# Kernel tuning notes

Measured on AMD Instinct MI355X. Metric: run time of the kernel, lower is better.

Reference implementation:

```python
import jax, jax.numpy as jnp
import numpy as np

GN_GROUPS = 32
GN_EPS = 1e-5


def _conv3x3(x, w, b):
    # NCHW 3x3 conv, stride 1, pad 1
    y = jax.lax.conv_general_dilated(x, w, (1, 1), [(1, 1), (1, 1)],
                                     dimension_numbers=('NCHW', 'OIHW', 'NCHW'))
    return y + b[None, :, None, None]


def _bilinear(x, py, px):
    # x: [N,C,H,W]; py,px: [N,H,W] fractional sample coords; zeros outside.
    N, C, H, W = x.shape
    y0 = jnp.floor(py)
    x0 = jnp.floor(px)
    wy = py - y0
    wx = px - x0
    xf = x.reshape(N, C, H * W)
    out = jnp.zeros((N, C, H, W), x.dtype)
    corners = ((y0, x0, (1 - wy) * (1 - wx)),
               (y0, x0 + 1, (1 - wy) * wx),
               (y0 + 1, x0, wy * (1 - wx)),
               (y0 + 1, x0 + 1, wy * wx))
    for yy, xx, w in corners:
        valid = ((yy >= 0) & (yy <= H - 1) & (xx >= 0) & (xx <= W - 1)).astype(x.dtype)
        yi = jnp.clip(yy, 0, H - 1).astype(jnp.int32)
        xi = jnp.clip(xx, 0, W - 1).astype(jnp.int32)
        idx = (yi * W + xi).reshape(N, 1, H * W)
        g = jnp.take_along_axis(xf, idx, axis=2).reshape(N, C, H, W)
        out = out + g * (w * valid)[:, None]
    return out


def setup_inputs() -> dict:
    key = jax.random.key(0)
    ks = jax.random.split(key, 8)
    N, C, H, W = 4, 128, 160, 160
    s = 0.05
    return {
        'x': jax.random.normal(ks[0], (N, C, H, W), jnp.float32),
        'w_tm': jax.random.normal(ks[1], (4, C, 3, 3), jnp.float32) * s,
        'b_tm': jax.random.normal(ks[2], (4,), jnp.float32) * s,
        'w_tr': jax.random.normal(ks[3], (2, C, 3, 3), jnp.float32) * s,
        'b_tr': jax.random.normal(ks[4], (2,), jnp.float32) * s,
        'w_dcn': jax.random.normal(ks[5], (C, C, 3, 3), jnp.float32) * s,
        'gn_gamma': jnp.ones((C,), jnp.float32),
        'gn_beta': jnp.zeros((C,), jnp.float32),
    }


def reference(x, w_tm, b_tm, w_tr, b_tr, w_dcn, gn_gamma, gn_beta):
    N, C, H, W = x.shape
    Cout = w_dcn.shape[0]
    # regular 3x3 grid offsets: row0 = ky, row1 = kx, k ordered ky-major
    R = jnp.array([[-1., -1., -1., 0., 0., 0., 1., 1., 1.],
                   [-1., 0., 1., -1., 0., 1., -1., 0., 1.]], x.dtype)
    tm = _conv3x3(x, w_tm, b_tm)   # [N,4,H,W] -> per-pixel 2x2 affine
    tr = _conv3x3(x, w_tr, b_tr)   # [N,2,H,W] -> per-pixel (dy,dx) translation
    tmm = tm.transpose(0, 2, 3, 1).reshape(N, H, W, 2, 2)
    off = jnp.einsum('nhwij,jk->nhwik', tmm, R) - R  # [N,H,W,2,9]
    dy = off[:, :, :, 0, :] + tr[:, 0][..., None]    # [N,H,W,9]
    dx = off[:, :, :, 1, :] + tr[:, 1][..., None]
    hh = jnp.arange(H, dtype=x.dtype)[None, :, None, None]
    ww = jnp.arange(W, dtype=x.dtype)[None, None, :, None]
    kk = jnp.arange(9)
    ky = (kk // 3).astype(x.dtype)
    kx = (kk % 3).astype(x.dtype)
    py = hh - 1.0 + ky + dy  # stride=1, pad=1, dilation=1
    px = ww - 1.0 + kx + dx
    wk = w_dcn.reshape(Cout, C, 9)
    out = jnp.zeros((N, Cout, H, W), x.dtype)
    for k in range(9):  # fixed small loop over kernel points
        s = _bilinear(x, py[..., k], px[..., k])
        out = out + jnp.einsum('nchw,oc->nohw', s, wk[:, :, k])
    # GroupNorm
    og = out.reshape(N, GN_GROUPS, (Cout // GN_GROUPS) * H * W)
    mu = og.mean(axis=2, keepdims=True)
    var = og.var(axis=2, keepdims=True)
    og = (og - mu) * jax.lax.rsqrt(var + GN_EPS)
    out = og.reshape(N, Cout, H, W) * gn_gamma[None, :, None, None] + gn_beta[None, :, None, None]
    return jax.nn.relu(out + x)
```

## Files before the change

### kernel.cpp

```cpp
#include <hip/hip_runtime.h>
#include <hip/hip_fp16.h>
#include <math.h>

#define Hh 160
#define Ww 160
#define Cc 128
#define HW 25600
#define NPIX 102400

typedef __attribute__((ext_vector_type(8))) _Float16 half8;
typedef __attribute__((ext_vector_type(4))) float f32x4;
typedef __attribute__((ext_vector_type(4))) unsigned int u32x4;

union h2u { __half2 h; unsigned int u; };

#define WS_OFFS 0u
#define WS_WA   7372800u
#define WS_GSUM 7667712u
#define WS_GSQ  7668224u
#define WS_XT   7668736u
#define WS_RAW  33883136u

__global__ void wtrans_kernel(const float* __restrict__ w_dcn,
                              unsigned short* __restrict__ wA) {
    int idx = blockIdx.x * 256 + threadIdx.x;
    if (idx >= 9 * 128 * 128) return;
    int k = idx >> 14;
    int o = (idx >> 7) & 127;
    int c = idx & 127;
    wA[idx] = __half_as_ushort(__float2half(w_dcn[(o * 128 + c) * 9 + k]));
}

__global__ void __launch_bounds__(256) xpose_kernel(
    const float* __restrict__ x, unsigned short* __restrict__ xT) {
    __shared__ float L[128 * 65];
    int b = blockIdx.x;
    int n = b / 400;
    int px0 = (b - n * 400) * 64;
    int t = threadIdx.x;
    const float* xn = x + (size_t)n * Cc * HW + px0;
#pragma unroll
    for (int i = 0; i < 32; ++i) {
        int idx = i * 256 + t;
        int ch = idx >> 6;
        int pxl = idx & 63;
        L[ch * 65 + pxl] = xn[(size_t)ch * HW + pxl];
    }
    __syncthreads();
    unsigned short* dst = xT + ((size_t)n * HW + px0) * 128;
#pragma unroll
    for (int j = 0; j < 16; ++j) {
        int idx = j * 256 + t;
        int pxl = idx >> 6;
        int cp = idx & 63;
        h2u cv;
        cv.h = __floats2half2_rn(L[(2 * cp) * 65 + pxl],
                                 L[(2 * cp + 1) * 65 + pxl]);
        *(unsigned int*)(dst + (size_t)pxl * 128 + cp * 2) = cv.u;
    }
}

__global__ void __launch_bounds__(256) offs_kernel(
    const float* __restrict__ x, const float* __restrict__ w_tm,
    const float* __restrict__ b_tm, const float* __restrict__ w_tr,
    const float* __restrict__ b_tr, float* __restrict__ offs2) {
    __shared__ float wt[128 * 9 * 8];
    int t = threadIdx.x;
    for (int idx = t; idx < 6912; idx += 256) {
        int j = idx % 6;
        int rest = idx / 6;
        int tap = rest % 9;
        int c = rest / 9;
        float v = (j < 4) ? w_tm[(j * 128 + c) * 9 + tap]
                          : w_tr[((j - 4) * 128 + c) * 9 + tap];
        wt[rest * 8 + j] = v;
    }
    __syncthreads();
    int bid = blockIdx.x;
    int blk = (bid & 7) * 50 + (bid >> 3);
    int p = blk * 256 + t;
    int n = p / HW;
    int hw = p - n * HW;
    int h = hw / Ww;
    int w = hw - h * Ww;
    int addr[9];
    float msk[9];
#pragma unroll
    for (int tap = 0; tap < 9; ++tap) {
        int dy = tap / 3 - 1, dx = tap % 3 - 1;
        int yy = h + dy, xx = w + dx;
        bool v = (yy >= 0) && (yy < Hh) && (xx >= 0) && (xx < Ww);
        addr[tap] = v ? yy * Ww + xx : 0;
        msk[tap] = v ? 1.f : 0.f;
    }
    float a0 = 0, a1 = 0, a2 = 0, a3 = 0, a4 = 0, a5 = 0;
    const float* xn = x + n * Cc * HW;
#pragma unroll 2
    for (int c = 0; c < Cc; ++c) {
        const float* xc = xn + c * HW;
#pragma unroll
        for (int tap = 0; tap < 9; ++tap) {
            float v = msk[tap] * xc[addr[tap]];
            const float* wp = &wt[(c * 9 + tap) * 8];
            float4 w4 = *(const float4*)wp;
            float2 w2 = *(const float2*)(wp + 4);
            a0 += v * w4.x; a1 += v * w4.y; a2 += v * w4.z; a3 += v * w4.w;
            a4 += v * w2.x; a5 += v * w2.y;
        }
    }
    a0 += b_tm[0]; a1 += b_tm[1]; a2 += b_tm[2]; a3 += b_tm[3];
    a4 += b_tr[0]; a5 += b_tr[1];
#pragma unroll
    for (int k = 0; k < 9; ++k) {
        float r0 = (float)(k / 3) - 1.f;
        float r1 = (float)(k % 3) - 1.f;
        float2 st;
        st.x = (float)h + a0 * r0 + a1 * r1 + a4;
        st.y = (float)w + a2 * r0 + a3 * r1 + a5;
        *(float2*)(offs2 + ((size_t)k * NPIX + p) * 2) = st;
    }
}

__global__ void __launch_bounds__(256, 3) dcn2_kernel(
    const unsigned short* __restrict__ xT, const float* __restrict__ offs2,
    const unsigned short* __restrict__ wA, float* __restrict__ raw,
    float* __restrict__ gsum, float* __restrict__ gsq) {
    __shared__ __align__(16) unsigned short Bt[128 * 128];
    int t = threadIdx.x;
    int lane = t & 63;
    int wid = t >> 6;
    int wm = wid & 1, wn = wid >> 1;
    int quad = lane >> 4, l15 = lane & 15;
    int sub = lane >> 4;
    int s = lane & 15;

    int bid = blockIdx.x;
    int blk = (bid & 7) * 100 + (bid >> 3);
    int px0 = blk * 128;
    int n = px0 / HW;
    int hw0 = px0 - n * HW;
    const unsigned short* xb = xT + (size_t)n * HW * 128;
    const char* Ag = (const char*)wA;

    f32x4 acc[4][4];
#pragma unroll
    for (int i = 0; i < 4; ++i)
#pragma unroll
        for (int j = 0; j < 4; ++j) acc[i][j] = (f32x4)0.f;

    for (int k = 0; k < 9; ++k) {
        __syncthreads();
#pragma unroll 2
        for (int r = 0; r < 8; ++r) {
            int p = wid * 32 + r * 4 + sub;
            const float2 pc = *(const float2*)(offs2 +
                                ((size_t)k * NPIX + px0 + p) * 2);
            float py = pc.x, pxx = pc.y;
            float y0f = floorf(py), x0f = floorf(pxx);
            float fy = py - y0f, fx = pxx - x0f;
            int y0 = (int)y0f, xi0 = (int)x0f;
            int y1 = y0 + 1, xi1 = xi0 + 1;
            float w00 = (1.f - fy) * (1.f - fx), w01 = (1.f - fy) * fx;
            float w10 = fy * (1.f - fx), w11 = fy * fx;
            bool vy0 = (unsigned)y0 < (unsigned)Hh;
            bool vy1 = (unsigned)y1 < (unsigned)Hh;
            bool vx0 = (unsigned)xi0 < (unsigned)Ww;
            bool vx1 = (unsigned)xi1 < (unsigned)Ww;
            w00 = (vy0 && vx0) ? w00 : 0.f;
            w01 = (vy0 && vx1) ? w01 : 0.f;
            w10 = (vy1 && vx0) ? w10 : 0.f;
            w11 = (vy1 && vx1) ? w11 : 0.f;
            int cy0 = vy0 ? y0 : 0, cy1 = vy1 ? y1 : 0;
            int cx0 = vx0 ? xi0 : 0, cx1 = vx1 ? xi1 : 0;
            int sb = s << 3;
            u32x4 v00 = *(const u32x4*)(xb + ((size_t)(cy0 * Ww + cx0) << 7) + sb);
            u32x4 v01 = *(const u32x4*)(xb + ((size_t)(cy0 * Ww + cx1) << 7) + sb);
            u32x4 v10 = *(const u32x4*)(xb + ((size_t)(cy1 * Ww + cx0) << 7) + sb);
            u32x4 v11 = *(const u32x4*)(xb + ((size_t)(cy1 * Ww + cx1) << 7) + sb);
            __half2 W00 = __float2half2_rn(w00);
            __half2 W01 = __float2half2_rn(w01);
            __half2 W10 = __float2half2_rn(w10);
            __half2 W11 = __float2half2_rn(w11);
            u32x4 outv;
#pragma unroll
            for (int e = 0; e < 4; ++e) {
                h2u a, b, c, d, o;
                a.u = v00[e]; b.u = v01[e]; c.u = v10[e]; d.u = v11[e];
                __half2 acc2 = __hmul2(W11, d.h);
                acc2 = __hfma2(W10, c.h, acc2);
                acc2 = __hfma2(W01, b.h, acc2);
                acc2 = __hfma2(W00, a.h, acc2);
                o.h = acc2;
                outv[e] = o.u;
            }
            *(u32x4*)&Bt[p * 128 + ((s ^ (p & 15)) << 3)] = outv;
        }
        __syncthreads();

#pragma unroll
        for (int q = 0; q < 4; ++q) {
            half8 a[4], b[4];
#pragma unroll
            for (int i = 0; i < 4; ++i)
                a[i] = *(const half8*)(Ag +
                        ((size_t)(k * 128 + wm * 64 + i * 16 + l15) << 8) +
                        q * 64 + quad * 16);
#pragma unroll
            for (int j = 0; j < 4; ++j) {
                int row = wn * 64 + j * 16 + l15;
                int ur = (q * 4 + quad) ^ (row & 15);
                b[j] = *(const half8*)&Bt[row * 128 + ur * 8];
            }
#pragma unroll
            for (int i = 0; i < 4; ++i)
#pragma unroll
                for (int j = 0; j < 4; ++j)
                    acc[i][j] = __builtin_amdgcn_mfma_f32_16x16x32_f16(
                        a[i], b[j], acc[i][j], 0, 0, 0);
        }
    }

    size_t rbase = ((size_t)n * Cc) * HW + hw0;
#pragma unroll
    for (int i = 0; i < 4; ++i) {
        float s_i = 0.f, q_i = 0.f;
#pragma unroll
        for (int j = 0; j < 4; ++j) {
            int pxl = wn * 64 + j * 16 + l15;
#pragma unroll
            for (int rr = 0; rr < 4; ++rr) {
                int o = wm * 64 + i * 16 + quad * 4 + rr;
                float v = acc[i][j][rr];
                raw[rbase + (size_t)o * HW + pxl] = v;
                s_i += v;
                q_i += v * v;
            }
        }
#pragma unroll
        for (int m = 1; m < 16; m <<= 1) {
            s_i += __shfl_xor(s_i, m);
            q_i += __shfl_xor(q_i, m);
        }
        if (l15 == 0) {
            int g = wm * 16 + i * 4 + quad;
            atomicAdd(&gsum[n * 32 + g], s_i);
            atomicAdd(&gsq[n * 32 + g], q_i);
        }
    }
}

__global__ void __launch_bounds__(256) finish_kernel(
    const float* __restrict__ raw, const float* __restrict__ x,
    const float* __restrict__ gsum, const float* __restrict__ gsq,
    const float* __restrict__ gamma, const float* __restrict__ beta,
    float* __restrict__ out) {
    int i = blockIdx.x * 256 + threadIdx.x;
    int e = i * 4;
    int n = e / (Cc * HW);
    int rem = e - n * (Cc * HW);
    int c = rem / HW;
    int g = c >> 2;
    const float inv = 1.f / 102400.f;
    float mu = gsum[n * 32 + g] * inv;
    float var = gsq[n * 32 + g] * inv - mu * mu;
    float rs = rsqrtf(var + 1e-5f);
    float sc = gamma[c] * rs;
    float sh = beta[c] - mu * sc;
    float4 v = *(const float4*)&raw[e];
    float4 xv = *(const float4*)&x[e];
    float4 r;
    r.x = fmaxf(v.x * sc + sh + xv.x, 0.f);
    r.y = fmaxf(v.y * sc + sh + xv.y, 0.f);
    r.z = fmaxf(v.z * sc + sh + xv.z, 0.f);
    r.w = fmaxf(v.w * sc + sh + xv.w, 0.f);
    *(float4*)&out[e] = r;
}

extern "C" void kernel_launch(void* const* d_in, const int* in_sizes, int n_in,
                              void* d_out, int out_size, void* d_ws, size_t ws_size,
                              hipStream_t stream) {
    const float* x      = (const float*)d_in[0];
    const float* w_tm   = (const float*)d_in[1];
    const float* b_tm   = (const float*)d_in[2];
    const float* w_tr   = (const float*)d_in[3];
    const float* b_tr   = (const float*)d_in[4];
    const float* w_dcn  = (const float*)d_in[5];
    const float* gamma  = (const float*)d_in[6];
    const float* beta   = (const float*)d_in[7];
    char* ws = (char*)d_ws;
    float*          offs2 = (float*)(ws + WS_OFFS);
    unsigned short* wA    = (unsigned short*)(ws + WS_WA);
    float*          gsum  = (float*)(ws + WS_GSUM);
    float*          gsq   = (float*)(ws + WS_GSQ);
    unsigned short* xT    = (unsigned short*)(ws + WS_XT);
    float*          raw   = (float*)(ws + WS_RAW);
    float* out = (float*)d_out;

    (void)hipMemsetAsync(gsum, 0, 1024, stream);
    wtrans_kernel<<<576, 256, 0, stream>>>(w_dcn, wA);
    xpose_kernel<<<1600, 256, 0, stream>>>(x, xT);
    offs_kernel<<<400, 256, 0, stream>>>(x, w_tm, b_tm, w_tr, b_tr, offs2);
    dcn2_kernel<<<800, 256, 0, stream>>>(xT, offs2, wA, raw, gsum, gsq);
    finish_kernel<<<12800, 256, 0, stream>>>(raw, x, gsum, gsq, gamma, beta, out);
}
```

Before: 358.5 us.

## Use MFMA for offset convs and register-resident B fragments in DCN

```diff
diff --git a/kernel.cpp b/kernel.cpp
--- a/kernel.cpp
+++ b/kernel.cpp
@@ -13,17 +13,32 @@
 typedef __attribute__((ext_vector_type(4))) unsigned int u32x4;
 
 union h2u { __half2 h; unsigned int u; };
-
-#define WS_OFFS 0u
-#define WS_WA   7372800u
-#define WS_GSUM 7667712u
-#define WS_GSQ  7668224u
-#define WS_XT   7668736u
-#define WS_RAW  33883136u
+union v16 { u32x4 u; half8 h; };
+
+#define WS_OFFS  0u
+#define WS_WA    7372800u
+#define WS_WP16  7667712u
+#define WS_GSUM  7704576u
+#define WS_GSQ   7705088u
+#define WS_XT    7705600u
+#define WS_RAW   33920000u
 
 __global__ void wtrans_kernel(const float* __restrict__ w_dcn,
-                              unsigned short* __restrict__ wA) {
+                              const float* __restrict__ w_tm,
+                              const float* __restrict__ w_tr,
+                              unsigned short* __restrict__ wA,
+                              unsigned short* __restrict__ wP16) {
     int idx = blockIdx.x * 256 + threadIdx.x;
+    if (idx < 16 * 1152) {
+        int m = idx / 1152;
+        int r = idx - m * 1152;
+        int tap = r >> 7;
+        int c = r & 127;
+        float v = 0.f;
+        if (m < 4) v = w_tm[(m * 128 + c) * 9 + tap];
+        else if (m < 6) v = w_tr[((m - 4) * 128 + c) * 9 + tap];
+        wP16[idx] = __half_as_ushort(__float2half(v));
+    }
     if (idx >= 9 * 128 * 128) return;
     int k = idx >> 14;
     int o = (idx >> 7) & 127;
@@ -61,63 +76,62 @@
 }
 
 __global__ void __launch_bounds__(256) offs_kernel(
-    const float* __restrict__ x, const float* __restrict__ w_tm,
-    const float* __restrict__ b_tm, const float* __restrict__ w_tr,
-    const float* __restrict__ b_tr, float* __restrict__ offs2) {
-    __shared__ float wt[128 * 9 * 8];
+    const unsigned short* __restrict__ xT, const unsigned short* __restrict__ wP16,
+    const float* __restrict__ b_tm, const float* __restrict__ b_tr,
+    float* __restrict__ offs2) {
     int t = threadIdx.x;
-    for (int idx = t; idx < 6912; idx += 256) {
-        int j = idx % 6;
-        int rest = idx / 6;
-        int tap = rest % 9;
-        int c = rest / 9;
-        float v = (j < 4) ? w_tm[(j * 128 + c) * 9 + tap]
-                          : w_tr[((j - 4) * 128 + c) * 9 + tap];
-        wt[rest * 8 + j] = v;
-    }
-    __syncthreads();
+    int lane = t & 63, wid = t >> 6;
+    int quad = lane >> 4, l15 = lane & 15;
     int bid = blockIdx.x;
-    int blk = (bid & 7) * 50 + (bid >> 3);
-    int p = blk * 256 + t;
-    int n = p / HW;
-    int hw = p - n * HW;
+    int blk = (bid & 7) * 200 + (bid >> 3);
+    int pxb = blk * 64 + wid * 16;
+    int n = pxb / HW;
+    int hw0 = pxb - n * HW;
+    int hw = hw0 + l15;
     int h = hw / Ww;
     int w = hw - h * Ww;
-    int addr[9];
-    float msk[9];
+    const char* xb = (const char*)(xT + (size_t)n * HW * 128);
+    const char* Wp = (const char*)wP16;
+    f32x4 acc = (f32x4)0.f;
 #pragma unroll
     for (int tap = 0; tap < 9; ++tap) {
         int dy = tap / 3 - 1, dx = tap % 3 - 1;
         int yy = h + dy, xx = w + dx;
-        bool v = (yy >= 0) && (yy < Hh) && (xx >= 0) && (xx < Ww);
-        addr[tap] = v ? yy * Ww + xx : 0;
-        msk[tap] = v ? 1.f : 0.f;
-    }
-    float a0 = 0, a1 = 0, a2 = 0, a3 = 0, a4 = 0, a5 = 0;
-    const float* xn = x + n * Cc * HW;
-#pragma unroll 2
-    for (int c = 0; c < Cc; ++c) {
-        const float* xc = xn + c * HW;
-#pragma unroll
-        for (int tap = 0; tap < 9; ++tap) {
-            float v = msk[tap] * xc[addr[tap]];
-            const float* wp = &wt[(c * 9 + tap) * 8];
-            float4 w4 = *(const float4*)wp;
-            float2 w2 = *(const float2*)(wp + 4);
-            a0 += v * w4.x; a1 += v * w4.y; a2 += v * w4.z; a3 += v * w4.w;
-            a4 += v * w2.x; a5 += v * w2.y;
-        }
-    }
-    a0 += b_tm[0]; a1 += b_tm[1]; a2 += b_tm[2]; a3 += b_tm[3];
-    a4 += b_tr[0]; a5 += b_tr[1];
-#pragma unroll
-    for (int k = 0; k < 9; ++k) {
-        float r0 = (float)(k / 3) - 1.f;
-        float r1 = (float)(k % 3) - 1.f;
-        float2 st;
-        st.x = (float)h + a0 * r0 + a1 * r1 + a4;
-        st.y = (float)w + a2 * r0 + a3 * r1 + a5;
-        *(float2*)(offs2 + ((size_t)k * NPIX + p) * 2) = st;
+        bool valid = ((unsigned)yy < (unsigned)Hh) && ((unsigned)xx < (unsigned)Ww);
+        int cell = (valid ? yy : 0) * Ww + (valid ? xx : 0);
+        __half2 m2 = __float2half2_rn(valid ? 1.f : 0.f);
+        const char* cbp = xb + ((size_t)cell << 8) + quad * 16;
+#pragma unroll
+        for (int q = 0; q < 4; ++q) {
+            v16 bv;
+            bv.u = *(const u32x4*)(cbp + q * 64);
+#pragma unroll
+            for (int e = 0; e < 4; ++e) {
+                h2u xv; xv.u = bv.u[e];
+                xv.h = __hmul2(xv.h, m2);
+                bv.u[e] = xv.u;
+            }
+            half8 av = *(const half8*)(Wp +
+                        ((size_t)l15 * 1152 + tap * 128 + q * 32 + quad * 8) * 2);
+            acc = __builtin_amdgcn_mfma_f32_16x16x32_f16(av, bv.h, acc, 0, 0, 0);
+        }
+    }
+    float a4 = __shfl(acc[0], 16 + l15);
+    float a5 = __shfl(acc[1], 16 + l15);
+    if (quad == 0) {
+        int p = pxb + l15;
+        float a0 = acc[0] + b_tm[0], a1 = acc[1] + b_tm[1];
+        float a2 = acc[2] + b_tm[2], a3 = acc[3] + b_tm[3];
+        a4 += b_tr[0]; a5 += b_tr[1];
+#pragma unroll
+        for (int k = 0; k < 9; ++k) {
+            float r0 = (float)(k / 3) - 1.f;
+            float r1 = (float)(k % 3) - 1.f;
+            float2 st;
+            st.x = (float)h + a0 * r0 + a1 * r1 + a4;
+            st.y = (float)w + a2 * r0 + a3 * r1 + a5;
+            *(float2*)(offs2 + ((size_t)k * NPIX + p) * 2) = st;
+        }
     }
 }
 
@@ -125,127 +139,123 @@
     const unsigned short* __restrict__ xT, const float* __restrict__ offs2,
     const unsigned short* __restrict__ wA, float* __restrict__ raw,
     float* __restrict__ gsum, float* __restrict__ gsq) {
-    __shared__ __align__(16) unsigned short Bt[128 * 128];
+    __shared__ float red[4][64];
     int t = threadIdx.x;
-    int lane = t & 63;
-    int wid = t >> 6;
-    int wm = wid & 1, wn = wid >> 1;
+    int lane = t & 63, wid = t >> 6;
     int quad = lane >> 4, l15 = lane & 15;
-    int sub = lane >> 4;
-    int s = lane & 15;
-
     int bid = blockIdx.x;
     int blk = (bid & 7) * 100 + (bid >> 3);
-    int px0 = blk * 128;
-    int n = px0 / HW;
-    int hw0 = px0 - n * HW;
-    const unsigned short* xb = xT + (size_t)n * HW * 128;
+    int px0b = blk * 128;
+    int n = px0b / HW;
+    int hw0 = px0b - n * HW + wid * 32;
+    int px0 = px0b + wid * 32;
+    const char* xb = (const char*)(xT + (size_t)n * HW * 128);
     const char* Ag = (const char*)wA;
 
-    f32x4 acc[4][4];
-#pragma unroll
-    for (int i = 0; i < 4; ++i)
-#pragma unroll
-        for (int j = 0; j < 4; ++j) acc[i][j] = (f32x4)0.f;
-
+    f32x4 acc[8][2];
+#pragma unroll
+    for (int i = 0; i < 8; ++i) {
+        acc[i][0] = (f32x4)0.f;
+        acc[i][1] = (f32x4)0.f;
+    }
+
+#pragma unroll 1
     for (int k = 0; k < 9; ++k) {
-        __syncthreads();
-#pragma unroll 2
-        for (int r = 0; r < 8; ++r) {
-            int p = wid * 32 + r * 4 + sub;
-            const float2 pc = *(const float2*)(offs2 +
-                                ((size_t)k * NPIX + px0 + p) * 2);
-            float py = pc.x, pxx = pc.y;
-            float y0f = floorf(py), x0f = floorf(pxx);
-            float fy = py - y0f, fx = pxx - x0f;
+        const char* cb[2][4];
+        __half2 Wc[2][4];
+#pragma unroll
+        for (int j = 0; j < 2; ++j) {
+            int p = px0 + j * 16 + l15;
+            float2 pc = *(const float2*)(offs2 + ((size_t)k * NPIX + p) * 2);
+            float py = pc.x, px = pc.y;
+            float y0f = floorf(py), x0f = floorf(px);
+            float fy = py - y0f, fx = px - x0f;
             int y0 = (int)y0f, xi0 = (int)x0f;
             int y1 = y0 + 1, xi1 = xi0 + 1;
             float w00 = (1.f - fy) * (1.f - fx), w01 = (1.f - fy) * fx;
             float w10 = fy * (1.f - fx), w11 = fy * fx;
-            bool vy0 = (unsigned)y0 < (unsigned)Hh;
-            bool vy1 = (unsigned)y1 < (unsigned)Hh;
-            bool vx0 = (unsigned)xi0 < (unsigned)Ww;
-            bool vx1 = (unsigned)xi1 < (unsigned)Ww;
+            bool vy0 = (unsigned)y0 < (unsigned)Hh, vy1 = (unsigned)y1 < (unsigned)Hh;
+            bool vx0 = (unsigned)xi0 < (unsigned)Ww, vx1 = (unsigned)xi1 < (unsigned)Ww;
             w00 = (vy0 && vx0) ? w00 : 0.f;
             w01 = (vy0 && vx1) ? w01 : 0.f;
             w10 = (vy1 && vx0) ? w10 : 0.f;
             w11 = (vy1 && vx1) ? w11 : 0.f;
             int cy0 = vy0 ? y0 : 0, cy1 = vy1 ? y1 : 0;
             int cx0 = vx0 ? xi0 : 0, cx1 = vx1 ? xi1 : 0;
-            int sb = s << 3;
-            u32x4 v00 = *(const u32x4*)(xb + ((size_t)(cy0 * Ww + cx0) << 7) + sb);
-            u32x4 v01 = *(const u32x4*)(xb + ((size_t)(cy0 * Ww + cx1) << 7) + sb);
-            u32x4 v10 = *(const u32x4*)(xb + ((size_t)(cy1 * Ww + cx0) << 7) + sb);
-            u32x4 v11 = *(const u32x4*)(xb + ((size_t)(cy1 * Ww + cx1) << 7) + sb);
-            __half2 W00 = __float2half2_rn(w00);
-            __half2 W01 = __float2half2_rn(w01);
-            __half2 W10 = __float2half2_rn(w10);
-            __half2 W11 = __float2half2_rn(w11);
-            u32x4 outv;
+            cb[j][0] = xb + ((size_t)(cy0 * Ww + cx0) << 8) + quad * 16;
+            cb[j][1] = xb + ((size_t)(cy0 * Ww + cx1) << 8) + quad * 16;
+            cb[j][2] = xb + ((size_t)(cy1 * Ww + cx0) << 8) + quad * 16;
+            cb[j][3] = xb + ((size_t)(cy1 * Ww + cx1) << 8) + quad * 16;
+            Wc[j][0] = __float2half2_rn(w00);
+            Wc[j][1] = __float2half2_rn(w01);
+            Wc[j][2] = __float2half2_rn(w10);
+            Wc[j][3] = __float2half2_rn(w11);
+        }
+        v16 b[2][4];
+#pragma unroll
+        for (int q = 0; q < 4; ++q)
+#pragma unroll
+            for (int j = 0; j < 2; ++j) {
+                u32x4 v0 = *(const u32x4*)(cb[j][0] + q * 64);
+                u32x4 v1 = *(const u32x4*)(cb[j][1] + q * 64);
+                u32x4 v2 = *(const u32x4*)(cb[j][2] + q * 64);
+                u32x4 v3 = *(const u32x4*)(cb[j][3] + q * 64);
+#pragma unroll
+                for (int e = 0; e < 4; ++e) {
+                    h2u A, B, C, D, O;
+                    A.u = v0[e]; B.u = v1[e]; C.u = v2[e]; D.u = v3[e];
+                    __half2 r = __hmul2(Wc[j][3], D.h);
+                    r = __hfma2(Wc[j][2], C.h, r);
+                    r = __hfma2(Wc[j][1], B.h, r);
+                    r = __hfma2(Wc[j][0], A.h, r);
+                    O.h = r;
+                    b[j][q].u[e] = O.u;
+                }
+            }
+#pragma unroll
+        for (int q = 0; q < 4; ++q) {
+            int koff = ((k * 128 + l15) << 8) + q * 64 + quad * 16;
+#pragma unroll
+            for (int i = 0; i < 8; ++i) {
+                half8 av = *(const half8*)(Ag + koff + (i << 12));
+                acc[i][0] = __builtin_amdgcn_mfma_f32_16x16x32_f16(
+                    av, b[0][q].h, acc[i][0], 0, 0, 0);
+                acc[i][1] = __builtin_amdgcn_mfma_f32_16x16x32_f16(
+                    av, b[1][q].h, acc[i][1], 0, 0, 0);
+            }
+        }
+    }
+
+    size_t rbase = ((size_t)n * Cc) * HW + hw0;
+#pragma unroll
+    for (int i = 0; i < 8; ++i) {
+        float s_i = 0.f, q_i = 0.f;
+#pragma unroll
+        for (int j = 0; j < 2; ++j)
 #pragma unroll
             for (int e = 0; e < 4; ++e) {
-                h2u a, b, c, d, o;
-                a.u = v00[e]; b.u = v01[e]; c.u = v10[e]; d.u = v11[e];
-                __half2 acc2 = __hmul2(W11, d.h);
-                acc2 = __hfma2(W10, c.h, acc2);
-                acc2 = __hfma2(W01, b.h, acc2);
-                acc2 = __hfma2(W00, a.h, acc2);
-                o.h = acc2;
-                outv[e] = o.u;
-            }
-            *(u32x4*)&Bt[p * 128 + ((s ^ (p & 15)) << 3)] = outv;
-        }
-        __syncthreads();
-
-#pragma unroll
-        for (int q = 0; q < 4; ++q) {
-            half8 a[4], b[4];
-#pragma unroll
-            for (int i = 0; i < 4; ++i)
-                a[i] = *(const half8*)(Ag +
-                        ((size_t)(k * 128 + wm * 64 + i * 16 + l15) << 8) +
-                        q * 64 + quad * 16);
-#pragma unroll
-            for (int j = 0; j < 4; ++j) {
-                int row = wn * 64 + j * 16 + l15;
-                int ur = (q * 4 + quad) ^ (row & 15);
-                b[j] = *(const half8*)&Bt[row * 128 + ur * 8];
-            }
-#pragma unroll
-            for (int i = 0; i < 4; ++i)
-#pragma unroll
-                for (int j = 0; j < 4; ++j)
-                    acc[i][j] = __builtin_amdgcn_mfma_f32_16x16x32_f16(
-                        a[i], b[j], acc[i][j], 0, 0, 0);
-        }
-    }
-
-    size_t rbase = ((size_t)n * Cc) * HW + hw0;
-#pragma unroll
-    for (int i = 0; i < 4; ++i) {
-        float s_i = 0.f, q_i = 0.f;
-#pragma unroll
-        for (int j = 0; j < 4; ++j) {
-            int pxl = wn * 64 + j * 16 + l15;
-#pragma unroll
-            for (int rr = 0; rr < 4; ++rr) {
-                int o = wm * 64 + i * 16 + quad * 4 + rr;
-                float v = acc[i][j][rr];
-                raw[rbase + (size_t)o * HW + pxl] = v;
+                int o = i * 16 + quad * 4 + e;
+                float v = acc[i][j][e];
+                raw[rbase + (size_t)o * HW + j * 16 + l15] = v;
                 s_i += v;
                 q_i += v * v;
             }
-        }
 #pragma unroll
         for (int m = 1; m < 16; m <<= 1) {
             s_i += __shfl_xor(s_i, m);
             q_i += __shfl_xor(q_i, m);
         }
         if (l15 == 0) {
-            int g = wm * 16 + i * 4 + quad;
-            atomicAdd(&gsum[n * 32 + g], s_i);
-            atomicAdd(&gsq[n * 32 + g], q_i);
-        }
+            red[wid][i * 4 + quad] = s_i;
+            red[wid][32 + i * 4 + quad] = q_i;
+        }
+    }
+    __syncthreads();
+    if (t < 64) {
+        float tot = red[0][t] + red[1][t] + red[2][t] + red[3][t];
+        int g = t & 31;
+        if (t < 32) atomicAdd(&gsum[n * 32 + g], tot);
+        else        atomicAdd(&gsq[n * 32 + g], tot);
     }
 }
 
@@ -290,6 +300,7 @@
     char* ws = (char*)d_ws;
     float*          offs2 = (float*)(ws + WS_OFFS);
     unsigned short* wA    = (unsigned short*)(ws + WS_WA);
+    unsigned short* wP16  = (unsigned short*)(ws + WS_WP16);
     float*          gsum  = (float*)(ws + WS_GSUM);
     float*          gsq   = (float*)(ws + WS_GSQ);
     unsigned short* xT    = (unsigned short*)(ws + WS_XT);
@@ -297,9 +308,9 @@
     float* out = (float*)d_out;
 
     (void)hipMemsetAsync(gsum, 0, 1024, stream);
-    wtrans_kernel<<<576, 256, 0, stream>>>(w_dcn, wA);
+    wtrans_kernel<<<576, 256, 0, stream>>>(w_dcn, w_tm, w_tr, wA, wP16);
     xpose_kernel<<<1600, 256, 0, stream>>>(x, xT);
-    offs_kernel<<<400, 256, 0, stream>>>(x, w_tm, b_tm, w_tr, b_tr, offs2);
+    offs_kernel<<<1600, 256, 0, stream>>>(xT, wP16, b_tm, b_tr, offs2);
     dcn2_kernel<<<800, 256, 0, stream>>>(xT, offs2, wA, raw, gsum, gsq);
     finish_kernel<<<12800, 256, 0, stream>>>(raw, x, gsum, gsq, gamma, beta, out);
 }
```

Measured after the change: 478.3 us. +33.4%, slower.
